# Kernel tuning notes

Hardware: AMD Instinct MI355X
Metric: run time of the kernel (lower is better)

Reference implementation:

```python
import jax, jax.numpy as jnp
import numpy as np

B, IMG, CIN, COUT = 8, 256, 64, 64
TILE_NUM, KSIZE = 4, 5
TILE = IMG // TILE_NUM                 # 64
FFT = KSIZE + TILE - 1                 # 68
PAD = (FFT - TILE) // 2                # 2


def setup_inputs() -> dict:
    key = jax.random.key(0)
    kx, kk = jax.random.split(key)
    x = jax.random.normal(kx, (B, IMG, IMG, CIN), dtype=jnp.float32)
    # build(): spatial random kernel -> fft2d -> trainable real/imag parts
    kernel_init = jax.random.normal(kk, (COUT, CIN, FFT, FFT), dtype=jnp.float32)
    kernel_fft = jnp.fft.fft2(kernel_init.astype(jnp.complex64))
    kernel_real = jnp.real(kernel_fft).astype(jnp.float32)
    kernel_imag = jnp.imag(kernel_fft).astype(jnp.float32)
    bias = jnp.zeros((COUT,), dtype=jnp.float32)
    return {"x": x, "kernel_real": kernel_real, "kernel_imag": kernel_imag, "bias": bias}


def _stitch(parts, pad, axis):
    """Overlap-add concat of tiles along `axis` with `pad` overlapping pixels."""
    parts = [jnp.moveaxis(p, axis, -1) for p in parts]
    out = parts[0]
    for p in parts[1:]:
        out = jnp.concatenate(
            [out[..., :-pad], out[..., -pad:] + p[..., :pad], p[..., pad:]], axis=-1)
    return jnp.moveaxis(out, -1, axis)


def reference(x, kernel_real, kernel_imag, bias):
    # x: [B, H, W, Cin] NHWC. Extract non-overlapping TILE x TILE tiles
    # (extract_glimpse centered at tile centers == plain tiling).
    b = x.shape[0]
    tiles = x.reshape(b, TILE_NUM, TILE, TILE_NUM, TILE, CIN)
    tiles = tiles.transpose(0, 1, 3, 5, 2, 4)            # [B, tr, tc, Cin, T, T]
    # pad_to_bounding_box: place tile at (PAD, PAD) inside FFT x FFT canvas
    tiles = jnp.pad(tiles, ((0, 0), (0, 0), (0, 0), (0, 0), (PAD, PAD), (PAD, PAD)))
    tiles_fft = jnp.fft.fft2(tiles.astype(jnp.complex64))  # [B, tr, tc, Cin, F, F]
    kfreq = jax.lax.complex(kernel_real, kernel_imag)      # [Cout, Cin, F, F]
    # complex multiply + reduce over input channels
    out_fft = jnp.einsum('brcihw,oihw->brcohw', tiles_fft, kfreq)
    out_tiles = jnp.real(jnp.fft.ifft2(out_fft)) + bias[:, None, None]  # [B,tr,tc,Cout,F,F]
    # overlap-add stitch: columns (last axis) then rows (axis -2)
    rows = [_stitch([out_tiles[:, r, c] for c in range(TILE_NUM)], PAD, axis=-1)
            for r in range(TILE_NUM)]
    full = _stitch(rows, PAD, axis=-2)                     # [B, Cout, Hs, Ws]
    full = full.transpose(0, 2, 3, 1)                      # NHWC
    return full[:, :IMG, :IMG, :]                          # crop_to_bounding_box(0,0,IMG,IMG)
```

## Files before the change

### kernel.cpp

```cpp
#include <hip/hip_runtime.h>
#include <hip/hip_bf16.h>


#define KH   35
#define CHS  4874240ull
#define KTB_FLOATS 9748480ull
#define WS_HEAD 34456ull

typedef float f32x4 __attribute__((ext_vector_type(4)));
typedef short s16x8 __attribute__((ext_vector_type(8)));

__device__ __forceinline__ ushort f2bf(float f) {
    __hip_bfloat16 h = __float2bfloat16(f);
    return *reinterpret_cast<ushort*>(&h);
}
__device__ __forceinline__ uint pkbf(float re, float im) {
    return (uint)f2bf(re) | ((uint)f2bf(im) << 16);
}

__global__ void k_twiddle(float* ws) {
    const float TWO_PI = 6.28318530717958647692f;
    int t = threadIdx.x;
    ushort* Wfb = (ushort*)(ws + 13976);
    for (int e = t; e < 80 * 64; e += 256) {
        int k = e >> 6, r = e & 63;
        float vr = 0.f, vi = 0.f;
        if (k < 68) {
            int ph = (k * (r + 2)) % 68;
            float a = TWO_PI * (float)ph / 68.0f;
            vr = cosf(a); vi = -sinf(a);
        }
        Wfb[e]        = f2bf(vr);
        Wfb[5120 + e] = f2bf(vi);
    }
    ushort* Wib = (ushort*)(ws + 19096);
    for (int e = t; e < 80 * 96; e += 256) {
        int p = e / 96, k = e % 96;
        float vr = 0.f, vi = 0.f;
        if (p < 68 && k < 68) {
            int ph = (p * k) % 68;
            float a = TWO_PI * (float)ph / 68.0f;
            vr = cosf(a) / 68.0f; vi = sinf(a) / 68.0f;
        }
        int dst = p * 128 + (((k >> 3) ^ (p & 7)) << 3) + (k & 7);
        Wib[dst]         = f2bf(vr);
        Wib[10240 + dst] = f2bf(vi);
    }
    ushort* Wgb = (ushort*)(ws + 29336);
    for (int e = t; e < 80 * 96; e += 256) {
        int q = e / 96, k = e % 96;
        float v = 0.f;
        if (q < 68 && k < 70) {
            int k2 = (k < KH) ? k : (k - KH);
            int ph = (q * k2) % 68;
            float a = TWO_PI * (float)ph / 68.0f;
            float alpha = (k2 == 0 || k2 == 34) ? 1.0f : 2.0f;
            v = (k < KH) ? (alpha * cosf(a) / 68.0f)
                         : (-alpha * sinf(a) / 68.0f);
        }
        int dst = q * 128 + (((k >> 3) ^ (q & 7)) << 3) + (k & 7);
        Wgb[dst] = f2bf(v);
    }
}

__global__ void k_zero_seams(float* out) {
    int b = blockIdx.x / 12, line = blockIdx.x % 12;
    const int seam[6] = {66, 67, 132, 133, 198, 199};
    int t = threadIdx.x;
    if (line < 6) {
        int y = seam[line];
        float4* dst = (float4*)(out + ((size_t)(b * 256 + y)) * 256 * 64);
        for (int e = t; e < 4096; e += 256) dst[e] = make_float4(0, 0, 0, 0);
    } else {
        int x = seam[line - 6];
        float4* dst = (float4*)out;
        for (int e = t; e < 4096; e += 256) {
            int y = e >> 4, f = e & 15;
            dst[(((size_t)(b * 256 + y)) * 256 + x) * 16 + f] = make_float4(0, 0, 0, 0);
        }
    }
}

__global__ __launch_bounds__(256) void k_kprep(
        const float* __restrict__ kr, const float* __restrict__ ki,
        ushort* __restrict__ Ktb) {
    __shared__ float tr[2 * 64 * KH];
    __shared__ float ti[2 * 64 * KH];
    int k1 = blockIdx.x >> 5, opr = blockIdx.x & 31;
    int t = threadIdx.x;
    int h = t >> 7;
    int rem = t & 127;
    int op = rem >> 6, i = rem & 63;
    int o = opr * 2 + op;
    const float* srcR = kr + ((size_t)(o * 64 + i) * 68 + k1) * 68;
    const float* srcI = ki + ((size_t)(o * 64 + i) * 68 + k1) * 68;
    float* tR = tr + (op * 64 + i) * KH;
    float* tI = ti + (op * 64 + i) * KH;
    #pragma unroll
    for (int j = 0; j < 4; ++j) {
        int k0 = (h * 4 + j) * 4;
        float4 v = *(const float4*)(srcR + k0);
        float4 w = *(const float4*)(srcI + k0);
        tR[k0] = v.x; tR[k0 + 1] = v.y; tR[k0 + 2] = v.z; tR[k0 + 3] = v.w;
        tI[k0] = w.x; tI[k0 + 1] = w.y; tI[k0 + 2] = w.z; tI[k0 + 3] = w.w;
    }
    if (h) {
        float2 v2 = *(const float2*)(srcR + 32);
        float2 w2 = *(const float2*)(srcI + 32);
        tR[32] = v2.x; tR[33] = v2.y; tR[34] = srcR[34];
        tI[32] = w2.x; tI[33] = w2.y; tI[34] = srcI[34];
    }
    __syncthreads();
    for (int e = t; e < KH * 128; e += 256) {
        int k2 = e >> 7, rem2 = e & 127;
        int op2 = rem2 >> 6, i2 = rem2 & 63;
        int o2 = opr * 2 + op2;
        int sw = (((i2 >> 3) ^ (o2 & 7)) << 3) + (i2 & 7);
        size_t base = ((size_t)(k1 * KH + k2)) * 8192 + (size_t)o2 * 64 + sw;
        Ktb[base]        = f2bf(tr[(op2 * 64 + i2) * KH + k2]);
        Ktb[base + 4096] = f2bf(ti[(op2 * 64 + i2) * KH + k2]);
    }
}

__global__ __launch_bounds__(512) void k_fwd_row(
        const float* __restrict__ x, const ushort* __restrict__ Wfb,
        uint* __restrict__ Y, int c0) {
    __shared__ __align__(16) ushort sAr[48 * 64];
    __shared__ __align__(16) ushort sAi[48 * 64];
    __shared__ __align__(16) ushort sB[4 * 64 * 64];
    int gid = blockIdx.x;
    int lc = gid >> 8;
    int rem = gid & 255;
    int nl = rem >> 4, rq = rem & 15;
    int n = (c0 + lc) * 16 + nl;
    int b = n >> 4, tr = (n >> 2) & 3, tc = n & 3;
    int t = threadIdx.x;
    for (int e = t; e < 3072; e += 512) {
        int m = e >> 6, c = e & 63;
        int sw = (m << 6) + (((c >> 3) ^ (m & 7)) << 3) + (c & 7);
        sAr[sw] = Wfb[e];
        sAi[sw] = Wfb[5120 + e];
    }
    for (int e = t; e < 4096; e += 512) {
        int rr = e >> 10, f = e & 1023;
        int c = f >> 4, i0 = (f & 15) << 2;
        int y = tr * 64 + rq * 4 + rr;
        const float4* src = (const float4*)(x + ((size_t)(b * 256 + y) * 256
                                                 + tc * 64) * 64 + (c << 6) + i0);
        float4 v = *src;
        float vv[4] = {v.x, v.y, v.z, v.w};
        #pragma unroll
        for (int u = 0; u < 4; ++u) {
            int i = i0 + u;
            sB[(rr << 12) + (i << 6) + (((c >> 3) ^ (i & 7)) << 3) + (c & 7)]
                = f2bf(vv[u]);
        }
    }
    __syncthreads();
    uint* Yc = Y + (size_t)lc * CHS;
    int lane = t & 63, w = t >> 6;
    int lm = lane & 15, kg = lane >> 4;
    int ba0 = ((kg ^ (lm & 7)) << 3);
    int ba1 = (((kg + 4) ^ (lm & 7)) << 3);
    for (int tid = w; tid < 48; tid += 8) {
        int rr = tid / 12, rem2 = tid % 12;
        int mt = rem2 >> 2, nt = rem2 & 3;
        int am = mt * 16 + lm, bn = nt * 16 + lm;
        s16x8 a0r = *(const s16x8*)(sAr + (am << 6) + ba0);
        s16x8 a1r = *(const s16x8*)(sAr + (am << 6) + ba1);
        s16x8 a0i = *(const s16x8*)(sAi + (am << 6) + ba0);
        s16x8 a1i = *(const s16x8*)(sAi + (am << 6) + ba1);
        s16x8 b0 = *(const s16x8*)(sB + (rr << 12) + (bn << 6) + ba0);
        s16x8 b1 = *(const s16x8*)(sB + (rr << 12) + (bn << 6) + ba1);
        f32x4 yr = {0.f, 0.f, 0.f, 0.f}, yi = yr;
        yr = __builtin_amdgcn_mfma_f32_16x16x32_bf16(a0r, b0, yr, 0, 0, 0);
        yr = __builtin_amdgcn_mfma_f32_16x16x32_bf16(a1r, b1, yr, 0, 0, 0);
        yi = __builtin_amdgcn_mfma_f32_16x16x32_bf16(a0i, b0, yi, 0, 0, 0);
        yi = __builtin_amdgcn_mfma_f32_16x16x32_bf16(a1i, b1, yi, 0, 0, 0);
        int r = rq * 4 + rr;
        #pragma unroll
        for (int g2 = 0; g2 < 4; ++g2) {
            int k2 = mt * 16 + kg * 4 + g2;
            if (k2 < KH)
                Yc[((size_t)(nl * KH + k2) * 64 + r) * 64 + nt * 16 + lm]
                    = pkbf(yr[g2], yi[g2]);
        }
    }
}

__global__ __launch_bounds__(512) void k_fwd_col(
        const uint* __restrict__ Y, const ushort* __restrict__ Wfb,
        uint* __restrict__ X) {
    __shared__ __align__(16) ushort sAr[80 * 64];
    __shared__ __align__(16) ushort sAi[80 * 64];
    __shared__ __align__(16) ushort sBr[64 * 64];
    __shared__ __align__(16) ushort sBi[64 * 64];
    int lc = blockIdx.x / 560;
    int rem = blockIdx.x % 560;
    int nl = rem / KH, k2 = rem % KH;
    const uint* Yg = Y + (size_t)lc * CHS + ((size_t)(nl * KH + k2)) * 4096;
    uint* Xc = X + (size_t)lc * CHS;
    int t = threadIdx.x;
    for (int e = t; e < 5120; e += 512) {
        int m = e >> 6, r = e & 63;
        int sw = (m << 6) + ((((r >> 3) ^ (m & 7))) << 3) + (r & 7);
        sAr[sw] = Wfb[e];
        sAi[sw] = Wfb[5120 + e];
    }
    for (int e = t; e < 4096; e += 512) {
        int i = e & 63, r = e >> 6;
        uint v = Yg[e];
        int sw = (i << 6) + ((((r >> 3) ^ (i & 7))) << 3) + (r & 7);
        sBr[sw] = (ushort)(v & 0xffff);
        sBi[sw] = (ushort)(v >> 16);
    }
    __syncthreads();
    int lane = t & 63, w = t >> 6;
    int lm = lane & 15, kg = lane >> 4;
    int ba0 = ((kg ^ (lm & 7)) << 3);
    int ba1 = (((kg + 4) ^ (lm & 7)) << 3);
    for (int tid = w; tid < 20; tid += 8) {
        int mt = tid >> 2, nt = tid & 3;
        int am = mt * 16 + lm, bn = nt * 16 + lm;
        s16x8 ar0 = *(const s16x8*)(sAr + (am << 6) + ba0);
        s16x8 ar1 = *(const s16x8*)(sAr + (am << 6) + ba1);
        s16x8 ai0 = *(const s16x8*)(sAi + (am << 6) + ba0);
        s16x8 ai1 = *(const s16x8*)(sAi + (am << 6) + ba1);
        s16x8 br0 = *(const s16x8*)(sBr + (bn << 6) + ba0);
        s16x8 br1 = *(const s16x8*)(sBr + (bn << 6) + ba1);
        s16x8 bi0 = *(const s16x8*)(sBi + (bn << 6) + ba0);
        s16x8 bi1 = *(const s16x8*)(sBi + (bn << 6) + ba1);
        f32x4 rr = {0.f, 0.f, 0.f, 0.f}, ii = rr, ri = rr, ir = rr;
        rr = __builtin_amdgcn_mfma_f32_16x16x32_bf16(ar0, br0, rr, 0, 0, 0);
        rr = __builtin_amdgcn_mfma_f32_16x16x32_bf16(ar1, br1, rr, 0, 0, 0);
        ii = __builtin_amdgcn_mfma_f32_16x16x32_bf16(ai0, bi0, ii, 0, 0, 0);
        ii = __builtin_amdgcn_mfma_f32_16x16x32_bf16(ai1, bi1, ii, 0, 0, 0);
        ri = __builtin_amdgcn_mfma_f32_16x16x32_bf16(ar0, bi0, ri, 0, 0, 0);
        ri = __builtin_amdgcn_mfma_f32_16x16x32_bf16(ar1, bi1, ri, 0, 0, 0);
        ir = __builtin_amdgcn_mfma_f32_16x16x32_bf16(ai0, br0, ir, 0, 0, 0);
        ir = __builtin_amdgcn_mfma_f32_16x16x32_bf16(ai1, br1, ir, 0, 0, 0);
        #pragma unroll
        for (int g2 = 0; g2 < 4; ++g2) {
            int k1 = mt * 16 + kg * 4 + g2;
            if (k1 < 68)
                Xc[((size_t)(nl * 68 + k1) * KH + k2) * 64 + nt * 16 + lm]
                    = pkbf(rr[g2] - ii[g2], ri[g2] + ir[g2]);
        }
    }
}

__global__ __launch_bounds__(256) void k_mix(
        const uint* __restrict__ X, const ushort* __restrict__ Ktb,
        uint* __restrict__ O, int CH) {
    __shared__ __align__(16) ushort sAr[16 * 64];
    __shared__ __align__(16) ushort sAi[16 * 64];
    __shared__ __align__(16) ushort sB[2 * 64 * 64];
    int bin = blockIdx.x / CH;
    int lc  = blockIdx.x % CH;
    int k1 = bin / KH, k2 = bin % KH;
    const uint* Xc = X + (size_t)lc * CHS;
    uint* Oc = O + (size_t)lc * CHS;
    int t = threadIdx.x;
    for (int e = t; e < 1024; e += 256) {
        int n = e >> 6, i = e & 63;
        uint v = Xc[((size_t)(n * 68 + k1) * KH + k2) * 64 + i];
        int sw = (n << 6) + (((i >> 3) ^ (n & 7)) << 3) + (i & 7);
        sAr[sw] = (ushort)(v & 0xffff);
        sAi[sw] = (ushort)(v >> 16);
    }
    const uint4* ksrc = (const uint4*)(Ktb + (size_t)bin * 8192);
    for (int e = t; e < 1024; e += 256) ((uint4*)sB)[e] = ksrc[e];
    __syncthreads();
    const ushort* sBr = sB;
    const ushort* sBi = sB + 4096;
    int lane = t & 63, w = t >> 6;
    int lm = lane & 15, kg = lane >> 4;
    f32x4 rr = {0.f, 0.f, 0.f, 0.f}, ii = rr, ri = rr, ir = rr;
    #pragma unroll
    for (int st = 0; st < 2; ++st) {
        int blk = kg + st * 4;
        int ao = (lm << 6) + ((blk ^ (lm & 7)) << 3);
        int bo = ((w * 16 + lm) << 6) + ((blk ^ (lm & 7)) << 3);
        s16x8 axr = *(const s16x8*)(sAr + ao);
        s16x8 axi = *(const s16x8*)(sAi + ao);
        s16x8 bxr = *(const s16x8*)(sBr + bo);
        s16x8 bxi = *(const s16x8*)(sBi + bo);
        rr = __builtin_amdgcn_mfma_f32_16x16x32_bf16(axr, bxr, rr, 0, 0, 0);
        ii = __builtin_amdgcn_mfma_f32_16x16x32_bf16(axi, bxi, ii, 0, 0, 0);
        ri = __builtin_amdgcn_mfma_f32_16x16x32_bf16(axr, bxi, ri, 0, 0, 0);
        ir = __builtin_amdgcn_mfma_f32_16x16x32_bf16(axi, bxr, ir, 0, 0, 0);
    }
    #pragma unroll
    for (int g2 = 0; g2 < 4; ++g2) {
        int n = kg * 4 + g2;
        int o = w * 16 + lm;
        Oc[(((size_t)n * KH + k2) * 68 + k1) * 64 + o]
            = pkbf(rr[g2] - ii[g2], ri[g2] + ir[g2]);
    }
}

__global__ __launch_bounds__(512) void k_inv_col(
        const uint* __restrict__ O, const ushort* __restrict__ Wib,
        uint* __restrict__ Z) {
    __shared__ __align__(16) ushort sAr[80 * 128];
    __shared__ __align__(16) ushort sAi[80 * 128];
    __shared__ __align__(16) ushort sBr[64 * 128];
    __shared__ __align__(16) ushort sBi[64 * 128];
    int lc = blockIdx.x / 560;
    int rem = blockIdx.x % 560;
    int nl = rem / KH, k2 = rem % KH;
    int t = threadIdx.x;
    const uint* Ob = O + (size_t)lc * CHS + ((size_t)nl * KH + k2) * 68 * 64;
    uint* Zc = Z + (size_t)lc * CHS;
    const uint4* wsrc = (const uint4*)Wib;
    for (int e = t; e < 1280; e += 512) ((uint4*)sAr)[e] = wsrc[e];
    for (int e = t; e < 1280; e += 512) ((uint4*)sAi)[e] = wsrc[1280 + e];
    uint4 zz = {0, 0, 0, 0};
    for (int e = t; e < 1024; e += 512) { ((uint4*)sBr)[e] = zz; ((uint4*)sBi)[e] = zz; }
    __syncthreads();
    for (int e = t; e < 4352; e += 512) {
        int k1 = e >> 6, o = e & 63;
        uint v = Ob[e];
        int sw = o * 128 + (((k1 >> 3) ^ (o & 7)) << 3) + (k1 & 7);
        sBr[sw] = (ushort)(v & 0xffff);
        sBi[sw] = (ushort)(v >> 16);
    }
    __syncthreads();
    int lane = t & 63, w = t >> 6;
    int lm = lane & 15, kg = lane >> 4;
    for (int tid = w; tid < 20; tid += 8) {
        int mt = tid >> 2, nt = tid & 3;
        int am = mt * 16 + lm, bn = nt * 16 + lm;
        f32x4 rr = {0.f, 0.f, 0.f, 0.f}, ii = rr, ri = rr, ir = rr;
        #pragma unroll
        for (int st = 0; st < 3; ++st) {
            int blk = kg + st * 4;
            int off = ((blk ^ (lm & 7)) << 3);
            s16x8 axr = *(const s16x8*)(sAr + am * 128 + off);
            s16x8 axi = *(const s16x8*)(sAi + am * 128 + off);
            s16x8 bxr = *(const s16x8*)(sBr + bn * 128 + off);
            s16x8 bxi = *(const s16x8*)(sBi + bn * 128 + off);
            rr = __builtin_amdgcn_mfma_f32_16x16x32_bf16(axr, bxr, rr, 0, 0, 0);
            ii = __builtin_amdgcn_mfma_f32_16x16x32_bf16(axi, bxi, ii, 0, 0, 0);
            ri = __builtin_amdgcn_mfma_f32_16x16x32_bf16(axr, bxi, ri, 0, 0, 0);
            ir = __builtin_amdgcn_mfma_f32_16x16x32_bf16(axi, bxr, ir, 0, 0, 0);
        }
        #pragma unroll
        for (int g2 = 0; g2 < 4; ++g2) {
            int p = mt * 16 + kg * 4 + g2;
            if (p < 68)
                Zc[(((size_t)(nl * 68 + p)) * KH + k2) * 64 + nt * 16 + lm]
                    = pkbf(rr[g2] - ii[g2], ri[g2] + ir[g2]);
        }
    }
}

__global__ __launch_bounds__(512) void k_fused_inv(
        const uint* __restrict__ Z, const ushort* __restrict__ Wgb,
        const float* __restrict__ bias, float* __restrict__ out, int c0) {
    __shared__ __align__(16) ushort sWg[80 * 128];
    __shared__ __align__(16) ushort sBq[2][64 * 128];
    int bid = blockIdx.x;
    int lc = bid / 272;
    int rem = bid % 272;
    int nl = rem / 17, pq = rem % 17;
    int b = c0 + lc;
    int tr = nl >> 2, tc = nl & 3;
    int t = threadIdx.x;
    const uint4* wsrc = (const uint4*)Wgb;
    for (int e = t; e < 1280; e += 512) ((uint4*)sWg)[e] = wsrc[e];
    uint4 zz = {0, 0, 0, 0};
    for (int e = t; e < 2048; e += 512) ((uint4*)sBq[0])[e] = zz;
    int lane = t & 63, w = t >> 6;
    int lm = lane & 15, kg = lane >> 4;
    float bv4[4];
    #pragma unroll
    for (int nt = 0; nt < 4; ++nt) bv4[nt] = bias[nt * 16 + lm];
    __syncthreads();
    for (int pp = 0; pp < 4; ++pp) {
        int p = pq * 4 + pp;
        int y = 66 * tr + p;
        if (y >= 256) break;
        ushort* Bq = sBq[pp & 1];
        const uint* Zb = Z + (size_t)lc * CHS + ((size_t)(nl * 68 + p)) * KH * 64;
        for (int e = t; e < KH * 64; e += 512) {
            int k2 = e >> 6, o = e & 63;
            uint v = Zb[e];
            int kb = k2 + KH;
            Bq[o * 128 + (((k2 >> 3) ^ (o & 7)) << 3) + (k2 & 7)] = (ushort)(v & 0xffff);
            Bq[o * 128 + (((kb >> 3) ^ (o & 7)) << 3) + (kb & 7)] = (ushort)(v >> 16);
        }
        __syncthreads();
        bool rowu = !((p <= 1 && tr > 0) || (p >= 66 && tr < 3));
        float* orow = out + ((size_t)(b * 256 + y)) * 256 * 64;
        for (int tid = w; tid < 20; tid += 8) {
            int mt = tid >> 2, nt = tid & 3;
            int am = mt * 16 + lm, bn = nt * 16 + lm;
            f32x4 acc = {0.f, 0.f, 0.f, 0.f};
            #pragma unroll
            for (int st = 0; st < 3; ++st) {
                int blk = kg + st * 4;
                int off = ((blk ^ (lm & 7)) << 3);
                s16x8 av = *(const s16x8*)(sWg + am * 128 + off);
                s16x8 bv = *(const s16x8*)(Bq + bn * 128 + off);
                acc = __builtin_amdgcn_mfma_f32_16x16x32_bf16(av, bv, acc, 0, 0, 0);
            }
            int o = nt * 16 + lm;
            #pragma unroll
            for (int g2 = 0; g2 < 4; ++g2) {
                int q = mt * 16 + kg * 4 + g2;
                if (q >= 68) continue;
                int xx = 66 * tc + q;
                if (xx >= 256) continue;
                bool colu = !((q <= 1 && tc > 0) || (q >= 66 && tc < 3));
                float v = acc[g2] + bv4[nt];
                float* addr = orow + (size_t)xx * 64 + o;
                if (rowu && colu) *addr = v;
                else              atomicAdd(addr, v);
            }
        }
    }
}

extern "C" void kernel_launch(void* const* d_in, const int* in_sizes, int n_in,
                              void* d_out, int out_size, void* d_ws, size_t ws_size,
                              hipStream_t stream) {
    const float* x    = (const float*)d_in[0];
    const float* kr   = (const float*)d_in[1];
    const float* ki   = (const float*)d_in[2];
    const float* bias = (const float*)d_in[3];
    float* out = (float*)d_out;
    float* ws  = (float*)d_ws;

    int CH = 8;
    while (CH > 4 && (WS_HEAD + KTB_FLOATS + 2ull * CH * CHS) * 4ull > ws_size)
        CH >>= 1;

    ushort* Wfb  = (ushort*)(ws + 13976);
    ushort* Wib  = (ushort*)(ws + 19096);
    ushort* Wgb  = (ushort*)(ws + 29336);
    ushort* Ktb  = (ushort*)(ws + WS_HEAD);
    float*  bufA = ws + WS_HEAD + KTB_FLOATS;
    float*  bufB = bufA + (size_t)CH * CHS;

    k_twiddle<<<1, 256, 0, stream>>>(ws);
    k_kprep<<<68 * 32, 256, 0, stream>>>(kr, ki, Ktb);
    k_zero_seams<<<96, 256, 0, stream>>>(out);

    for (int s = 0; s < 8; s += CH) {
        k_fwd_row<<<CH * 256, 512, 0, stream>>>(x, Wfb, (uint*)bufA, s);
        k_fwd_col<<<CH * 560, 512, 0, stream>>>((const uint*)bufA, Wfb, (uint*)bufB);
        k_mix<<<CH * 2380, 256, 0, stream>>>((const uint*)bufB, Ktb, (uint*)bufA, CH);
        k_inv_col<<<CH * 560, 512, 0, stream>>>((const uint*)bufA, Wib, (uint*)bufB);
        k_fused_inv<<<CH * 272, 512, 0, stream>>>((const uint*)bufB, Wgb, bias, out, s);
    }
}
```

Measured before the change: 382.6 us.

## Reuse per-bin kernel tile across chunk loop in mix kernel; one output channel per kprep block

The mix kernel now launches one block per frequency bin and loops over all CH chunks inside the block. The 16 KB bf16 kernel tile is loaded into shared memory once and reused, where before it was reloaded for every chunk. kprep is also split into one block per output channel with a smaller shared footprint and twice as many blocks. The trade-off is fewer mix blocks (2380 instead of CH×2380), with the work per chunk serialized by barriers, so latency hiding relies on occupancy.

```diff
diff --git a/kernel.cpp b/kernel.cpp
--- a/kernel.cpp
+++ b/kernel.cpp
@@ -84,41 +84,36 @@
 __global__ __launch_bounds__(256) void k_kprep(
         const float* __restrict__ kr, const float* __restrict__ ki,
         ushort* __restrict__ Ktb) {
-    __shared__ float tr[2 * 64 * KH];
-    __shared__ float ti[2 * 64 * KH];
-    int k1 = blockIdx.x >> 5, opr = blockIdx.x & 31;
-    int t = threadIdx.x;
-    int h = t >> 7;
-    int rem = t & 127;
-    int op = rem >> 6, i = rem & 63;
-    int o = opr * 2 + op;
+    __shared__ float tr[64 * KH];
+    __shared__ float ti[64 * KH];
+    int k1 = blockIdx.x >> 6, o = blockIdx.x & 63;
+    int t = threadIdx.x;
+    int i = t & 63, q = t >> 6;
     const float* srcR = kr + ((size_t)(o * 64 + i) * 68 + k1) * 68;
     const float* srcI = ki + ((size_t)(o * 64 + i) * 68 + k1) * 68;
-    float* tR = tr + (op * 64 + i) * KH;
-    float* tI = ti + (op * 64 + i) * KH;
+    float* tR = tr + i * KH;
+    float* tI = ti + i * KH;
     #pragma unroll
-    for (int j = 0; j < 4; ++j) {
-        int k0 = (h * 4 + j) * 4;
+    for (int s = 0; s < 2; ++s) {
+        int k0 = (q + 4 * s) * 4;
         float4 v = *(const float4*)(srcR + k0);
         float4 w = *(const float4*)(srcI + k0);
         tR[k0] = v.x; tR[k0 + 1] = v.y; tR[k0 + 2] = v.z; tR[k0 + 3] = v.w;
         tI[k0] = w.x; tI[k0 + 1] = w.y; tI[k0 + 2] = w.z; tI[k0 + 3] = w.w;
     }
-    if (h) {
+    if (q == 3) {
         float2 v2 = *(const float2*)(srcR + 32);
         float2 w2 = *(const float2*)(srcI + 32);
         tR[32] = v2.x; tR[33] = v2.y; tR[34] = srcR[34];
         tI[32] = w2.x; tI[33] = w2.y; tI[34] = srcI[34];
     }
     __syncthreads();
-    for (int e = t; e < KH * 128; e += 256) {
-        int k2 = e >> 7, rem2 = e & 127;
-        int op2 = rem2 >> 6, i2 = rem2 & 63;
-        int o2 = opr * 2 + op2;
-        int sw = (((i2 >> 3) ^ (o2 & 7)) << 3) + (i2 & 7);
-        size_t base = ((size_t)(k1 * KH + k2)) * 8192 + (size_t)o2 * 64 + sw;
-        Ktb[base]        = f2bf(tr[(op2 * 64 + i2) * KH + k2]);
-        Ktb[base + 4096] = f2bf(ti[(op2 * 64 + i2) * KH + k2]);
+    for (int e = t; e < KH * 64; e += 256) {
+        int k2 = e >> 6, i2 = e & 63;
+        int sw = (((i2 >> 3) ^ (o & 7)) << 3) + (i2 & 7);
+        size_t base = ((size_t)(k1 * KH + k2)) * 8192 + (size_t)o * 64 + sw;
+        Ktb[base]        = f2bf(tr[i2 * KH + k2]);
+        Ktb[base + 4096] = f2bf(ti[i2 * KH + k2]);
     }
 }
 
@@ -255,47 +250,49 @@
     __shared__ __align__(16) ushort sAr[16 * 64];
     __shared__ __align__(16) ushort sAi[16 * 64];
     __shared__ __align__(16) ushort sB[2 * 64 * 64];
-    int bin = blockIdx.x / CH;
-    int lc  = blockIdx.x % CH;
+    int bin = blockIdx.x;
     int k1 = bin / KH, k2 = bin % KH;
-    const uint* Xc = X + (size_t)lc * CHS;
-    uint* Oc = O + (size_t)lc * CHS;
-    int t = threadIdx.x;
-    for (int e = t; e < 1024; e += 256) {
-        int n = e >> 6, i = e & 63;
-        uint v = Xc[((size_t)(n * 68 + k1) * KH + k2) * 64 + i];
-        int sw = (n << 6) + (((i >> 3) ^ (n & 7)) << 3) + (i & 7);
-        sAr[sw] = (ushort)(v & 0xffff);
-        sAi[sw] = (ushort)(v >> 16);
-    }
+    int t = threadIdx.x;
     const uint4* ksrc = (const uint4*)(Ktb + (size_t)bin * 8192);
     for (int e = t; e < 1024; e += 256) ((uint4*)sB)[e] = ksrc[e];
-    __syncthreads();
     const ushort* sBr = sB;
     const ushort* sBi = sB + 4096;
     int lane = t & 63, w = t >> 6;
     int lm = lane & 15, kg = lane >> 4;
-    f32x4 rr = {0.f, 0.f, 0.f, 0.f}, ii = rr, ri = rr, ir = rr;
-    #pragma unroll
-    for (int st = 0; st < 2; ++st) {
-        int blk = kg + st * 4;
-        int ao = (lm << 6) + ((blk ^ (lm & 7)) << 3);
-        int bo = ((w * 16 + lm) << 6) + ((blk ^ (lm & 7)) << 3);
-        s16x8 axr = *(const s16x8*)(sAr + ao);
-        s16x8 axi = *(const s16x8*)(sAi + ao);
-        s16x8 bxr = *(const s16x8*)(sBr + bo);
-        s16x8 bxi = *(const s16x8*)(sBi + bo);
-        rr = __builtin_amdgcn_mfma_f32_16x16x32_bf16(axr, bxr, rr, 0, 0, 0);
-        ii = __builtin_amdgcn_mfma_f32_16x16x32_bf16(axi, bxi, ii, 0, 0, 0);
-        ri = __builtin_amdgcn_mfma_f32_16x16x32_bf16(axr, bxi, ri, 0, 0, 0);
-        ir = __builtin_amdgcn_mfma_f32_16x16x32_bf16(axi, bxr, ir, 0, 0, 0);
-    }
-    #pragma unroll
-    for (int g2 = 0; g2 < 4; ++g2) {
-        int n = kg * 4 + g2;
-        int o = w * 16 + lm;
-        Oc[(((size_t)n * KH + k2) * 68 + k1) * 64 + o]
-            = pkbf(rr[g2] - ii[g2], ri[g2] + ir[g2]);
+    for (int lc = 0; lc < CH; ++lc) {
+        const uint* Xc = X + (size_t)lc * CHS;
+        uint* Oc = O + (size_t)lc * CHS;
+        for (int e = t; e < 1024; e += 256) {
+            int n = e >> 6, i = e & 63;
+            uint v = Xc[((size_t)(n * 68 + k1) * KH + k2) * 64 + i];
+            int sw = (n << 6) + (((i >> 3) ^ (n & 7)) << 3) + (i & 7);
+            sAr[sw] = (ushort)(v & 0xffff);
+            sAi[sw] = (ushort)(v >> 16);
+        }
+        __syncthreads();
+        f32x4 rr = {0.f, 0.f, 0.f, 0.f}, ii = rr, ri = rr, ir = rr;
+        #pragma unroll
+        for (int st = 0; st < 2; ++st) {
+            int blk = kg + st * 4;
+            int ao = (lm << 6) + ((blk ^ (lm & 7)) << 3);
+            int bo = ((w * 16 + lm) << 6) + ((blk ^ (lm & 7)) << 3);
+            s16x8 axr = *(const s16x8*)(sAr + ao);
+            s16x8 axi = *(const s16x8*)(sAi + ao);
+            s16x8 bxr = *(const s16x8*)(sBr + bo);
+            s16x8 bxi = *(const s16x8*)(sBi + bo);
+            rr = __builtin_amdgcn_mfma_f32_16x16x32_bf16(axr, bxr, rr, 0, 0, 0);
+            ii = __builtin_amdgcn_mfma_f32_16x16x32_bf16(axi, bxi, ii, 0, 0, 0);
+            ri = __builtin_amdgcn_mfma_f32_16x16x32_bf16(axr, bxi, ri, 0, 0, 0);
+            ir = __builtin_amdgcn_mfma_f32_16x16x32_bf16(axi, bxr, ir, 0, 0, 0);
+        }
+        #pragma unroll
+        for (int g2 = 0; g2 < 4; ++g2) {
+            int n = kg * 4 + g2;
+            int o = w * 16 + lm;
+            Oc[(((size_t)n * KH + k2) * 68 + k1) * 64 + o]
+                = pkbf(rr[g2] - ii[g2], ri[g2] + ir[g2]);
+        }
+        __syncthreads();
     }
 }
 
@@ -444,13 +441,13 @@
     float*  bufB = bufA + (size_t)CH * CHS;
 
     k_twiddle<<<1, 256, 0, stream>>>(ws);
-    k_kprep<<<68 * 32, 256, 0, stream>>>(kr, ki, Ktb);
+    k_kprep<<<68 * 64, 256, 0, stream>>>(kr, ki, Ktb);
     k_zero_seams<<<96, 256, 0, stream>>>(out);
 
     for (int s = 0; s < 8; s += CH) {
         k_fwd_row<<<CH * 256, 512, 0, stream>>>(x, Wfb, (uint*)bufA, s);
         k_fwd_col<<<CH * 560, 512, 0, stream>>>((const uint*)bufA, Wfb, (uint*)bufB);
-        k_mix<<<CH * 2380, 256, 0, stream>>>((const uint*)bufB, Ktb, (uint*)bufA, CH);
+        k_mix<<<2380, 256, 0, stream>>>((const uint*)bufB, Ktb, (uint*)bufA, CH);
         k_inv_col<<<CH * 560, 512, 0, stream>>>((const uint*)bufA, Wib, (uint*)bufB);
         k_fused_inv<<<CH * 272, 512, 0, stream>>>((const uint*)bufB, Wgb, bias, out, s);
     }
```

New measurement: 361.4 us. -5.5%, faster.
